# Kernel tuning notes

Measured on AMD Instinct MI355X. Metric: run time of the kernel, lower is better.

## Reference

```python
import jax, jax.numpy as jnp
import numpy as np

B, N, C = 2, 384, 1024          # images, proposals/image, box_head feature dim
H_REPN = 256                    # RePN hidden
G_HID, HEADS = 256, 4           # GATConv hidden / heads
TOPK = 8
IMG_H, IMG_W = 800, 800
NEG_SLOPE = 0.2                 # PyG GATConv leaky_relu default


def _box_geom(bx):
    # normalized [x, y, w, h], matching _box_geom
    scale = jnp.array([IMG_W, IMG_H, IMG_W, IMG_H], dtype=bx.dtype)
    nb = bx / scale
    return jnp.stack([nb[:, 0], nb[:, 1], nb[:, 2] - nb[:, 0], nb[:, 3] - nb[:, 1]], axis=1)


def _gat_layer(x, src, tgt, W, att_src, att_dst, bias, heads, out_c):
    # PyG GATConv: messages flow src -> tgt, softmax over incoming edges at tgt
    n = x.shape[0]
    xw = (x @ W).reshape(n, heads, out_c)               # [N, H, F]
    a_s = jnp.sum(xw * att_src, axis=-1)                # [N, H]
    a_d = jnp.sum(xw * att_dst, axis=-1)                # [N, H]
    e = jax.nn.leaky_relu(a_s[src] + a_d[tgt], NEG_SLOPE)  # [E, H]
    e_max = jax.ops.segment_max(e, tgt, num_segments=n)    # stable softmax per target
    alpha = jnp.exp(e - e_max[tgt])
    denom = jax.ops.segment_sum(alpha, tgt, num_segments=n)
    alpha = alpha / jnp.maximum(denom, 1e-16)[tgt]          # [E, H]
    out = jax.ops.segment_sum(xw[src] * alpha[..., None], tgt, num_segments=n)
    return out.reshape(n, heads * out_c) + bias


def setup_inputs() -> dict:
    key = jax.random.key(0)
    ks = jax.random.split(key, 16)
    feats = jax.random.normal(ks[0], (B, N, C), dtype=jnp.float32)
    # boxes with x1<x2, y1<y2 inside the image
    xy = jax.random.uniform(ks[1], (B, N, 2), minval=0.0, maxval=650.0)
    wh = jax.random.uniform(ks[2], (B, N, 2), minval=10.0, maxval=150.0)
    boxes = jnp.concatenate([xy, xy + wh], axis=-1).astype(jnp.float32)
    s = 0.02
    params = {
        'fc1_w': jax.random.normal(ks[3], (2 * C + 4, H_REPN)) * s,
        'fc1_b': jnp.zeros((H_REPN,), jnp.float32),
        'fc2_w': jax.random.normal(ks[4], (H_REPN, 1)) * s,
        'fc2_b': jnp.zeros((1,), jnp.float32),
        'gat1_w': jax.random.normal(ks[5], (C + 4, HEADS * G_HID)) * s,
        'gat1_att_src': jax.random.normal(ks[6], (HEADS, G_HID)) * s,
        'gat1_att_dst': jax.random.normal(ks[7], (HEADS, G_HID)) * s,
        'gat1_b': jnp.zeros((HEADS * G_HID,), jnp.float32),
        'gat2_w': jax.random.normal(ks[8], (HEADS * G_HID, 2)) * s,
        'gat2_att_src': jax.random.normal(ks[9], (1, 2)) * s,
        'gat2_att_dst': jax.random.normal(ks[10], (1, 2)) * s,
        'gat2_b': jnp.zeros((2,), jnp.float32),
    }
    return {'feats': feats, 'boxes': boxes, **params}


def reference(feats, boxes, fc1_w, fc1_b, fc2_w, fc2_b,
              gat1_w, gat1_att_src, gat1_att_dst, gat1_b,
              gat2_w, gat2_att_src, gat2_att_dst, gat2_b):
    def single(f, bx):
        geom4 = _box_geom(bx)                               # [N, 4]
        x = jnp.concatenate([f, geom4], axis=1)             # [N, C+4]
        # RelationProposalNetwork: fc1(cat[f_i, f_j, |b_i-b_j|]) done as split matmuls
        Wa, Wb, Wg = fc1_w[:C], fc1_w[C:2 * C], fc1_w[2 * C:]
        p1 = f @ Wa                                         # [N, H]
        p2 = f @ Wb                                         # [N, H]
        gdiff = jnp.abs(bx[:, None, :] - bx[None, :, :])    # [N, N, 4]
        h = jax.nn.relu(p1[:, None, :] + p2[None, :, :] + gdiff @ Wg + fc1_b)
        rel = (h @ fc2_w)[..., 0] + fc2_b[0]                # [N, N]
        # _make_edge_index: mask diagonal, top-k per row; edge = [dst_node, neighbor]
        rn = rel - jnp.eye(N, dtype=rel.dtype) * 1e6
        nbr = jax.lax.top_k(rn, TOPK)[1]                    # [N, k]
        src = jnp.repeat(jnp.arange(N), TOPK)               # edge_index[0] (PyG source)
        tgt = nbr.reshape(-1)                               # edge_index[1] (PyG target)
        loop = jnp.arange(N)                                # GATConv add_self_loops=True
        src = jnp.concatenate([src, loop])
        tgt = jnp.concatenate([tgt, loop])
        h1 = jax.nn.relu(_gat_layer(x, src, tgt, gat1_w, gat1_att_src, gat1_att_dst, gat1_b, HEADS, G_HID))
        logits = _gat_layer(h1, src, tgt, gat2_w, gat2_att_src, gat2_att_dst, gat2_b, 1, 2)
        return logits                                       # [N, 2]
    return jax.vmap(single)(feats, boxes)
```

## Files before the change

### kernel.cpp

```cpp
#include <hip/hip_runtime.h>

#define BB 2
#define NN 384
#define CC 1024
#define HR 256
#define NHEADS 4
#define TOPK 8
#define CAP 448
#define NEG 0.2f

typedef __attribute__((ext_vector_type(8))) short bf16x8;
typedef __attribute__((ext_vector_type(4))) float f32x4;

__device__ __forceinline__ unsigned short f2bf(float v) {
    unsigned u = __float_as_uint(v);
    return (unsigned short)((u + 0x7FFFu + ((u >> 16) & 1u)) >> 16);
}
__device__ __forceinline__ float bf2f(unsigned short h) {
    return __uint_as_float((unsigned)h << 16);
}

__global__ __launch_bounds__(256) void k_prep(const float* __restrict__ feats,
        const float* __restrict__ boxes, const float* __restrict__ gat1_w,
        const float* __restrict__ fc1_w,
        uint4* __restrict__ Asw, uint4* __restrict__ Bsw,
        uint4* __restrict__ Ah, uint4* __restrict__ Al,
        uint4* __restrict__ Bh, uint4* __restrict__ Bl,
        float4* __restrict__ wgp, int* __restrict__ counts,
        float* __restrict__ xw2) {
    __shared__ float sw[32][65];
    int blk = blockIdx.x;
    int t = threadIdx.x;
    int gflat = blk * 256 + t;
    if (gflat < BB * NN) counts[gflat] = 0;
    if (gflat < BB * NN * 2) xw2[gflat] = 0.f;

    if (blk < 396) {
        int flat = gflat;
        int lane = flat & 63;
        int kc = (flat >> 6) % 33;
        int mt = flat / (33 * 64);
        int m = mt * 16 + (lane & 15);
        int k0 = kc * 32 + (lane >> 4) * 8;
        unsigned short vals[8];
        const float s = 1.0f / 800.0f;
#pragma unroll
        for (int j = 0; j < 8; j++) {
            int k = k0 + j;
            float v;
            if (k < CC) v = feats[(size_t)m * CC + k];
            else if (k < CC + 4) {
                const float* bx = boxes + (size_t)m * 4;
                int gk = k - CC;
                v = (gk == 0) ? bx[0] * s : (gk == 1) ? bx[1] * s
                  : (gk == 2) ? (bx[2] - bx[0]) * s : (bx[3] - bx[1]) * s;
            } else v = 0.f;
            vals[j] = f2bf(v);
        }
        uint4 pk;
        pk.x = (unsigned)vals[0] | ((unsigned)vals[1] << 16);
        pk.y = (unsigned)vals[2] | ((unsigned)vals[3] << 16);
        pk.z = (unsigned)vals[4] | ((unsigned)vals[5] << 16);
        pk.w = (unsigned)vals[6] | ((unsigned)vals[7] << 16);
        Asw[flat] = pk;
    } else if (blk < 924) {
        int blkrel = blk - 396;
        int ntg = blkrel / 33;
        int kc  = blkrel % 33;
        int k0 = kc * 32;
        int n0 = ntg * 64;
#pragma unroll
        for (int pass = 0; pass < 8; pass++) {
            int kl = pass * 4 + (t >> 6);
            int k = k0 + kl;
            int nl = t & 63;
            float v = (k < CC + 4) ? gat1_w[(size_t)k * 1024 + n0 + nl] : 0.f;
            sw[kl][nl] = v;
        }
        __syncthreads();
        int local_nt = t >> 6;
        int lane = t & 63;
        int nn = lane & 15;
        int q = lane >> 4;
        int nl = local_nt * 16 + nn;
        unsigned short vals[8];
#pragma unroll
        for (int j = 0; j < 8; j++) vals[j] = f2bf(sw[q * 8 + j][nl]);
        uint4 pk;
        pk.x = (unsigned)vals[0] | ((unsigned)vals[1] << 16);
        pk.y = (unsigned)vals[2] | ((unsigned)vals[3] << 16);
        pk.z = (unsigned)vals[4] | ((unsigned)vals[5] << 16);
        pk.w = (unsigned)vals[6] | ((unsigned)vals[7] << 16);
        int nt = ntg * 4 + local_nt;
        Bsw[(size_t)nt * 33 * 64 + kc * 64 + lane] = pk;
    } else if (blk < 1308) {
        int flat = gflat - 924 * 256;
        int lane = flat & 63;
        int kc = (flat >> 6) % 32;
        int mt = flat / (32 * 64);
        int m = mt * 16 + (lane & 15);
        int k0 = kc * 32 + (lane >> 4) * 8;
        unsigned short vh[8], vl[8];
        const float* src = feats + (size_t)m * CC + k0;
#pragma unroll
        for (int j = 0; j < 8; j++) {
            float v = src[j];
            unsigned short h = f2bf(v);
            vh[j] = h;
            vl[j] = f2bf(v - bf2f(h));
        }
        uint4 ph, pl;
        ph.x = (unsigned)vh[0] | ((unsigned)vh[1] << 16);
        ph.y = (unsigned)vh[2] | ((unsigned)vh[3] << 16);
        ph.z = (unsigned)vh[4] | ((unsigned)vh[5] << 16);
        ph.w = (unsigned)vh[6] | ((unsigned)vh[7] << 16);
        pl.x = (unsigned)vl[0] | ((unsigned)vl[1] << 16);
        pl.y = (unsigned)vl[2] | ((unsigned)vl[3] << 16);
        pl.z = (unsigned)vl[4] | ((unsigned)vl[5] << 16);
        pl.w = (unsigned)vl[6] | ((unsigned)vl[7] << 16);
        Ah[flat] = ph; Al[flat] = pl;
    } else if (blk < 1564) {
        int blkrel = blk - 1308;
        int ntg = blkrel / 32;
        int kc  = blkrel % 32;
        int k0 = kc * 32;
        int n0 = ntg * 64;
#pragma unroll
        for (int pass = 0; pass < 8; pass++) {
            int kl = pass * 4 + (t >> 6);
            int k = k0 + kl;
            int n = n0 + (t & 63);
            float v = (n < 256) ? fc1_w[(size_t)k * 256 + n]
                                : fc1_w[(size_t)(CC + k) * 256 + (n - 256)];
            sw[kl][t & 63] = v;
        }
        __syncthreads();
        int local_nt = t >> 6;
        int lane = t & 63;
        int nn = lane & 15;
        int q = lane >> 4;
        int nl = local_nt * 16 + nn;
        unsigned short vh[8], vl[8];
#pragma unroll
        for (int j = 0; j < 8; j++) {
            float v = sw[q * 8 + j][nl];
            unsigned short h = f2bf(v);
            vh[j] = h;
            vl[j] = f2bf(v - bf2f(h));
        }
        uint4 ph, pl;
        ph.x = (unsigned)vh[0] | ((unsigned)vh[1] << 16);
        ph.y = (unsigned)vh[2] | ((unsigned)vh[3] << 16);
        ph.z = (unsigned)vh[4] | ((unsigned)vh[5] << 16);
        ph.w = (unsigned)vh[6] | ((unsigned)vh[7] << 16);
        pl.x = (unsigned)vl[0] | ((unsigned)vl[1] << 16);
        pl.y = (unsigned)vl[2] | ((unsigned)vl[3] << 16);
        pl.z = (unsigned)vl[4] | ((unsigned)vl[5] << 16);
        pl.w = (unsigned)vl[6] | ((unsigned)vl[7] << 16);
        int nt = ntg * 4 + local_nt;
        size_t o = (size_t)nt * 32 * 64 + kc * 64 + lane;
        Bh[o] = ph; Bl[o] = pl;
    } else {
        int c = t;
        float4 w;
        w.x = fc1_w[(size_t)(2 * CC + 0) * HR + c];
        w.y = fc1_w[(size_t)(2 * CC + 1) * HR + c];
        w.z = fc1_w[(size_t)(2 * CC + 2) * HR + c];
        w.w = fc1_w[(size_t)(2 * CC + 3) * HR + c];
        wgp[c] = w;
    }
}

__global__ __launch_bounds__(512) void k_mm(const uint4* __restrict__ Ah,
        const uint4* __restrict__ Al, const uint4* __restrict__ Bh,
        const uint4* __restrict__ Bl, const float* __restrict__ fc1_b,
        float* __restrict__ p1, float* __restrict__ p2t,
        const uint4* __restrict__ Asw, const uint4* __restrict__ Bsw,
        float* __restrict__ xw1) {
    __shared__ float lds[4][64][8];
    int t = threadIdx.x;
    int w = t >> 6;
    int lane = t & 63;
    int g = w & 3;
    int kh = w >> 2;
    int blk0 = blockIdx.x;
    if (blk0 < 192) {
        int mtp = blk0 >> 3;
        int nt = (blk0 & 7) * 4 + g;
        int mt0 = mtp * 2;
        f32x4 acc0 = {0.f, 0.f, 0.f, 0.f};
        f32x4 acc1 = {0.f, 0.f, 0.f, 0.f};
        const uint4* pah0 = Ah + (size_t)mt0 * 32 * 64 + (size_t)kh * 16 * 64 + lane;
        const uint4* pal0 = Al + (size_t)mt0 * 32 * 64 + (size_t)kh * 16 * 64 + lane;
        const uint4* pbh = Bh + (size_t)nt * 32 * 64 + (size_t)kh * 16 * 64 + lane;
        const uint4* pbl = Bl + (size_t)nt * 32 * 64 + (size_t)kh * 16 * 64 + lane;
#pragma unroll 2
        for (int kc = 0; kc < 16; kc++) {
            uint4 ah0 = pah0[kc * 64];
            uint4 al0 = pal0[kc * 64];
            uint4 ah1 = pah0[kc * 64 + 2048];
            uint4 al1 = pal0[kc * 64 + 2048];
            uint4 bh = pbh[kc * 64];
            uint4 bl = pbl[kc * 64];
            acc0 = __builtin_amdgcn_mfma_f32_16x16x32_bf16(*(bf16x8*)&ah0, *(bf16x8*)&bh, acc0, 0, 0, 0);
            acc0 = __builtin_amdgcn_mfma_f32_16x16x32_bf16(*(bf16x8*)&ah0, *(bf16x8*)&bl, acc0, 0, 0, 0);
            acc0 = __builtin_amdgcn_mfma_f32_16x16x32_bf16(*(bf16x8*)&al0, *(bf16x8*)&bh, acc0, 0, 0, 0);
            acc1 = __builtin_amdgcn_mfma_f32_16x16x32_bf16(*(bf16x8*)&ah1, *(bf16x8*)&bh, acc1, 0, 0, 0);
            acc1 = __builtin_amdgcn_mfma_f32_16x16x32_bf16(*(bf16x8*)&ah1, *(bf16x8*)&bl, acc1, 0, 0, 0);
            acc1 = __builtin_amdgcn_mfma_f32_16x16x32_bf16(*(bf16x8*)&al1, *(bf16x8*)&bh, acc1, 0, 0, 0);
        }
        if (kh == 1) {
#pragma unroll
            for (int r = 0; r < 4; r++) { lds[g][lane][r] = acc0[r]; lds[g][lane][4 + r] = acc1[r]; }
        }
        __syncthreads();
        if (kh == 0) {
#pragma unroll
            for (int r = 0; r < 4; r++) { acc0[r] += lds[g][lane][r]; acc1[r] += lds[g][lane][4 + r]; }
            int col = nt * 16 + (lane & 15);
            int rbase = (lane >> 4) * 4;
            if (col < 256) {
                float bias = fc1_b[col];
#pragma unroll
                for (int r = 0; r < 4; r++) {
                    p1[(size_t)(mt0 * 16 + rbase + r) * 256 + col] = acc0[r] + bias;
                    p1[(size_t)(mt0 * 16 + 16 + rbase + r) * 256 + col] = acc1[r] + bias;
                }
            } else {
#pragma unroll
                for (int r = 0; r < 4; r++) {
                    int rr0 = mt0 * 16 + rbase + r;
                    int rr1 = rr0 + 16;
                    p2t[((size_t)(rr0 / NN) * 256 + (col - 256)) * NN + (rr0 % NN)] = acc0[r];
                    p2t[((size_t)(rr1 / NN) * 256 + (col - 256)) * NN + (rr1 % NN)] = acc1[r];
                }
            }
        }
    } else {
        int blk = blk0 - 192;
        int mtp = blk >> 4;
        int nt = (blk & 15) * 4 + g;
        int mt0 = mtp * 2;
        int nk = kh ? 16 : 17;
        f32x4 acc0 = {0.f, 0.f, 0.f, 0.f};
        f32x4 acc1 = {0.f, 0.f, 0.f, 0.f};
        const uint4* pa0 = Asw + (size_t)mt0 * 33 * 64 + (size_t)kh * 17 * 64 + lane;
        const uint4* pb = Bsw + (size_t)nt * 33 * 64 + (size_t)kh * 17 * 64 + lane;
#pragma unroll 4
        for (int kc = 0; kc < nk; kc++) {
            uint4 a0 = pa0[kc * 64];
            uint4 a1 = pa0[kc * 64 + 2112];
            uint4 bv = pb[kc * 64];
            acc0 = __builtin_amdgcn_mfma_f32_16x16x32_bf16(*(bf16x8*)&a0, *(bf16x8*)&bv, acc0, 0, 0, 0);
            acc1 = __builtin_amdgcn_mfma_f32_16x16x32_bf16(*(bf16x8*)&a1, *(bf16x8*)&bv, acc1, 0, 0, 0);
        }
        if (kh == 1) {
#pragma unroll
            for (int r = 0; r < 4; r++) { lds[g][lane][r] = acc0[r]; lds[g][lane][4 + r] = acc1[r]; }
        }
        __syncthreads();
        if (kh == 0) {
#pragma unroll
            for (int r = 0; r < 4; r++) { acc0[r] += lds[g][lane][r]; acc1[r] += lds[g][lane][4 + r]; }
            int col = nt * 16 + (lane & 15);
            int rbase = (lane >> 4) * 4;
#pragma unroll
            for (int r = 0; r < 4; r++) {
                xw1[(size_t)(mt0 * 16 + rbase + r) * 1024 + col] = acc0[r];
                xw1[(size_t)(mt0 * 16 + 16 + rbase + r) * 1024 + col] = acc1[r];
            }
        }
    }
}

__global__ __launch_bounds__(384) void k_relatt(const float* __restrict__ p1,
        const float* __restrict__ p2t, const float* __restrict__ boxes,
        const float4* __restrict__ wgp, const float* __restrict__ fc2_w,
        float* __restrict__ rel_a, float* __restrict__ rel_b,
        const float* __restrict__ xw1, const float* __restrict__ att_src,
        const float* __restrict__ att_dst, float* __restrict__ a_s,
        float* __restrict__ a_d) {
    int blk0 = blockIdx.x;
    if (blk0 < 768) {
        int blk = blk0;
        int p = blk >> 1;
        int ch = blk & 1;
        int b = p / (NN / 2);
        int i0 = (p - b * (NN / 2)) * 2;
        int row0 = b * NN + i0;
        int j = threadIdx.x;
        float a0 = boxes[(size_t)row0 * 4 + 0];
        float a1 = boxes[(size_t)row0 * 4 + 1];
        float a2 = boxes[(size_t)row0 * 4 + 2];
        float a3 = boxes[(size_t)row0 * 4 + 3];
        float c0 = boxes[(size_t)(row0 + 1) * 4 + 0];
        float c1 = boxes[(size_t)(row0 + 1) * 4 + 1];
        float c2 = boxes[(size_t)(row0 + 1) * 4 + 2];
        float c3 = boxes[(size_t)(row0 + 1) * 4 + 3];
        float4 bj = *(const float4*)(boxes + ((size_t)b * NN + j) * 4);
        float g00 = fabsf(a0 - bj.x), g01 = fabsf(a1 - bj.y);
        float g02 = fabsf(a2 - bj.z), g03 = fabsf(a3 - bj.w);
        float g10 = fabsf(c0 - bj.x), g11 = fabsf(c1 - bj.y);
        float g12 = fabsf(c2 - bj.z), g13 = fabsf(c3 - bj.w);
        const float* p1r0 = p1 + (size_t)row0 * HR + ch * 128;
        const float* p1r1 = p1r0 + HR;
        const float* p2b = p2t + (size_t)b * HR * NN + (size_t)ch * 128 * NN + j;
        const float4* wg = wgp + ch * 128;
        const float* w2 = fc2_w + ch * 128;
        float acc0 = 0.f, acc1 = 0.f;
#pragma unroll 8
        for (int c = 0; c < 128; c++) {
            float4 w = wg[c];
            float pa = p1r0[c];
            float pb = p1r1[c];
            float wc = w2[c];
            float p2v = p2b[(size_t)c * NN];
            float v0 = pa + p2v + g00 * w.x + g01 * w.y + g02 * w.z + g03 * w.w;
            float v1 = pb + p2v + g10 * w.x + g11 * w.y + g12 * w.z + g13 * w.w;
            acc0 += fmaxf(v0, 0.f) * wc;
            acc1 += fmaxf(v1, 0.f) * wc;
        }
        float* dst = ch ? rel_b : rel_a;
        dst[(size_t)row0 * NN + j] = acc0;
        dst[(size_t)(row0 + 1) * NN + j] = acc1;
    } else {
        int node = blk0 - 768;
        int t = threadIdx.x;
        if (t >= 256) return;
        int w = t >> 6;
        int lane = t & 63;
        const float4* xr = (const float4*)(xw1 + (size_t)node * 1024 + w * 256);
        const float4* sr = (const float4*)(att_src + w * 256);
        const float4* dr = (const float4*)(att_dst + w * 256);
        float4 x = xr[lane];
        float4 s = sr[lane];
        float4 d = dr[lane];
        float ps = x.x * s.x + x.y * s.y + x.z * s.z + x.w * s.w;
        float pd = x.x * d.x + x.y * d.y + x.z * d.z + x.w * d.w;
#pragma unroll
        for (int off = 32; off > 0; off >>= 1) {
            ps += __shfl_xor(ps, off);
            pd += __shfl_xor(pd, off);
        }
        if (lane == 0) {
            a_s[(size_t)node * NHEADS + w] = ps;
            a_d[(size_t)node * NHEADS + w] = pd;
        }
    }
}

__global__ __launch_bounds__(64) void k_topk_inv(const float* __restrict__ rel_a,
        const float* __restrict__ rel_b, int* __restrict__ counts,
        int* __restrict__ inlist) {
    int row = blockIdx.x;
    int b = row / NN;
    int i = row - b * NN;
    int t = threadIdx.x;
    const float* ra = rel_a + (size_t)row * NN;
    const float* rb = rel_b + (size_t)row * NN;
    float v[6]; int id[6];
#pragma unroll
    for (int q = 0; q < 6; q++) {
        int j = t + q * 64;
        float val = ra[j] + rb[j];
        if (j == i) val = -INFINITY;
        v[q] = val; id[q] = j;
    }
    int mine = -1;
    for (int k = 0; k < TOPK; k++) {
        float bv = -INFINITY; int bi = NN;
#pragma unroll
        for (int q = 0; q < 6; q++) {
            if (v[q] > bv || (v[q] == bv && id[q] < bi)) { bv = v[q]; bi = id[q]; }
        }
        for (int off = 32; off > 0; off >>= 1) {
            float ov = __shfl_down(bv, off);
            int   oi = __shfl_down(bi, off);
            if (ov > bv || (ov == bv && oi < bi)) { bv = ov; bi = oi; }
        }
        bi = __shfl(bi, 0);
        if (t == k) mine = bi;
#pragma unroll
        for (int q = 0; q < 6; q++) if (id[q] == bi) v[q] = -INFINITY;
    }
    if (t < TOPK) {
        int tg = b * NN + mine;
        int q = atomicAdd(&counts[tg], 1);
        inlist[(size_t)tg * CAP + q] = i;
    } else if (t == TOPK) {
        int q = atomicAdd(&counts[row], 1);
        inlist[(size_t)row * CAP + q] = i;
    }
}

__global__ __launch_bounds__(256) void k_agg1h(const int* __restrict__ counts,
        const int* __restrict__ inlist, const float* __restrict__ a_s,
        const float* __restrict__ a_d, const float* __restrict__ xw1,
        const float* __restrict__ gat1_b, const float* __restrict__ w2,
        float* __restrict__ xw2) {
    __shared__ int slist[CAP];
    __shared__ float walpha[CAP];
    __shared__ float redp[8];
    int blk = blockIdx.x;
    int node = blk >> 2;
    int h = blk & 3;
    int b = node / NN;
    int t = threadIdx.x;
    int wid = t >> 6;
    int lane = t & 63;
    int deg = counts[node];
    for (int e = t; e < deg; e += 256) slist[e] = inlist[(size_t)node * CAP + e];
    __syncthreads();
    if (t < 64) {
        float ad = a_d[(size_t)node * NHEADS + h];
        float vals[7];
        int cnt = 0;
        float vmax = -INFINITY;
        for (int e = t; e < deg; e += 64) {
            float x = a_s[(size_t)(b * NN + slist[e]) * NHEADS + h] + ad;
            x = x >= 0.f ? x : NEG * x;
            vals[cnt++] = x;
            vmax = fmaxf(vmax, x);
        }
#pragma unroll
        for (int off = 32; off > 0; off >>= 1)
            vmax = fmaxf(vmax, __shfl_xor(vmax, off));
        float sum = 0.f;
        for (int i = 0; i < cnt; i++) {
            vals[i] = expf(vals[i] - vmax);
            sum += vals[i];
        }
#pragma unroll
        for (int off = 32; off > 0; off >>= 1)
            sum += __shfl_xor(sum, off);
        float inv = 1.f / fmaxf(sum, 1e-16f);
        cnt = 0;
        for (int e = t; e < deg; e += 64) walpha[e] = vals[cnt++] * inv;
    }
    __syncthreads();
    float acc = 0.f;
    for (int e = 0; e < deg; e++)
        acc += walpha[e] * xw1[(size_t)(b * NN + slist[e]) * 1024 + h * 256 + t];
    float o = fmaxf(acc + gat1_b[h * 256 + t], 0.f);
    int d = h * 256 + t;
    float p0 = o * w2[d * 2];
    float p1v = o * w2[d * 2 + 1];
#pragma unroll
    for (int off = 32; off > 0; off >>= 1) {
        p0 += __shfl_xor(p0, off);
        p1v += __shfl_xor(p1v, off);
    }
    if (lane == 0) { redp[wid] = p0; redp[4 + wid] = p1v; }
    __syncthreads();
    if (t == 0) {
        atomicAdd(&xw2[(size_t)node * 2],     redp[0] + redp[1] + redp[2] + redp[3]);
        atomicAdd(&xw2[(size_t)node * 2 + 1], redp[4] + redp[5] + redp[6] + redp[7]);
    }
}

__global__ __launch_bounds__(64) void k_agg2(const int* __restrict__ counts,
        const int* __restrict__ inlist, const float* __restrict__ xw2,
        const float* __restrict__ as2, const float* __restrict__ ad2,
        const float* __restrict__ b2, float* __restrict__ out) {
    int node = blockIdx.x;
    int b = node / NN;
    int lane = threadIdx.x;
    int deg = counts[node];
    float s0 = as2[0], s1 = as2[1];
    float d0 = ad2[0], d1 = ad2[1];
    float2 xwn = *(const float2*)(xw2 + (size_t)node * 2);
    float ad = xwn.x * d0 + xwn.y * d1;
    float vals[7], xs0[7], xs1[7];
    int cnt = 0;
    float vmax = -INFINITY;
    for (int e = lane; e < deg; e += 64) {
        int s = b * NN + inlist[(size_t)node * CAP + e];
        float2 xws = *(const float2*)(xw2 + (size_t)s * 2);
        float x = xws.x * s0 + xws.y * s1 + ad;
        x = x >= 0.f ? x : NEG * x;
        xs0[cnt] = xws.x; xs1[cnt] = xws.y; vals[cnt] = x; cnt++;
        vmax = fmaxf(vmax, x);
    }
#pragma unroll
    for (int off = 32; off > 0; off >>= 1)
        vmax = fmaxf(vmax, __shfl_xor(vmax, off));
    float sum = 0.f;
    for (int i = 0; i < cnt; i++) {
        vals[i] = expf(vals[i] - vmax);
        sum += vals[i];
    }
#pragma unroll
    for (int off = 32; off > 0; off >>= 1)
        sum += __shfl_xor(sum, off);
    float inv = 1.f / fmaxf(sum, 1e-16f);
    float a0 = 0.f, a1 = 0.f;
    for (int i = 0; i < cnt; i++) {
        a0 += vals[i] * xs0[i];
        a1 += vals[i] * xs1[i];
    }
#pragma unroll
    for (int off = 32; off > 0; off >>= 1) {
        a0 += __shfl_xor(a0, off);
        a1 += __shfl_xor(a1, off);
    }
    if (lane == 0) {
        out[(size_t)node * 2]     = a0 * inv + b2[0];
        out[(size_t)node * 2 + 1] = a1 * inv + b2[1];
    }
}

extern "C" void kernel_launch(void* const* d_in, const int* in_sizes, int n_in,
                              void* d_out, int out_size, void* d_ws, size_t ws_size,
                              hipStream_t stream) {
    const float* feats  = (const float*)d_in[0];
    const float* boxes  = (const float*)d_in[1];
    const float* fc1_w  = (const float*)d_in[2];
    const float* fc1_b  = (const float*)d_in[3];
    const float* fc2_w  = (const float*)d_in[4];
    const float* fc2_b  = (const float*)d_in[5];
    const float* gat1_w = (const float*)d_in[6];
    const float* g1as   = (const float*)d_in[7];
    const float* g1ad   = (const float*)d_in[8];
    const float* gat1_b = (const float*)d_in[9];
    const float* gat2_w = (const float*)d_in[10];
    const float* g2as   = (const float*)d_in[11];
    const float* g2ad   = (const float*)d_in[12];
    const float* gat2_b = (const float*)d_in[13];
    float* out = (float*)d_out;
    (void)fc2_b;

    char* ws = (char*)d_ws;
    size_t off = 0;
    auto alloc = [&](size_t bytes) -> void* {
        void* p = ws + off;
        off += (bytes + 255) / 256 * 256;
        return p;
    };
    int*   counts = (int*)alloc((size_t)BB * NN * 4);
    int*   inlist = (int*)alloc((size_t)BB * NN * CAP * 4);
    float* p1     = (float*)alloc((size_t)BB * NN * HR * 4);
    float* p2t    = (float*)alloc((size_t)BB * HR * NN * 4);
    float* rel_a  = (float*)alloc((size_t)BB * NN * NN * 4);
    float* rel_b  = (float*)alloc((size_t)BB * NN * NN * 4);
    float* xw1    = (float*)alloc((size_t)BB * NN * 1024 * 4);
    float* a_s1   = (float*)alloc((size_t)BB * NN * NHEADS * 4);
    float* a_d1   = (float*)alloc((size_t)BB * NN * NHEADS * 4);
    float* xw2    = (float*)alloc((size_t)BB * NN * 2 * 4);
    uint4* Asw    = (uint4*)alloc((size_t)48 * 33 * 64 * 16);
    uint4* Bsw    = (uint4*)alloc((size_t)64 * 33 * 64 * 16);
    uint4* Ah     = (uint4*)alloc((size_t)48 * 32 * 64 * 16);
    uint4* Al     = (uint4*)alloc((size_t)48 * 32 * 64 * 16);
    uint4* Bh     = (uint4*)alloc((size_t)32 * 32 * 64 * 16);
    uint4* Bl     = (uint4*)alloc((size_t)32 * 32 * 64 * 16);
    float4* wgp   = (float4*)alloc((size_t)HR * 16);
    (void)ws_size; (void)in_sizes; (void)n_in; (void)out_size;

    k_prep<<<1565, 256, 0, stream>>>(feats, boxes, gat1_w, fc1_w,
                                     Asw, Bsw, Ah, Al, Bh, Bl, wgp, counts, xw2);
    k_mm<<<576, 512, 0, stream>>>(Ah, Al, Bh, Bl, fc1_b, p1, p2t, Asw, Bsw, xw1);
    k_relatt<<<1536, 384, 0, stream>>>(p1, p2t, boxes, wgp, fc2_w, rel_a, rel_b,
                                       xw1, g1as, g1ad, a_s1, a_d1);
    k_topk_inv<<<BB * NN, 64, 0, stream>>>(rel_a, rel_b, counts, inlist);
    k_agg1h<<<BB * NN * NHEADS, 256, 0, stream>>>(counts, inlist, a_s1, a_d1, xw1,
                                                  gat1_b, gat2_w, xw2);
    k_agg2<<<BB * NN, 64, 0, stream>>>(counts, inlist, xw2, g2as, g2ad, gat2_b, out);
}
```

Before: 161.6 us.

## Fuse relation scoring with per-row top-k selection and inverse edge list build

Merges the relation score kernel and the top-k kernel. Each block now computes both channel halves for two rows and runs a block-wide top-k using wave shuffles plus shared-memory reduction, then appends edges atomically. This removes the rel_a/rel_b global round trip and one kernel launch. In exchange, the relation blocks are halved in count and each does twice the serial work, and the top-k needs 16 block barriers per block, which reduces parallelism.

```diff
diff --git a/kernel.cpp b/kernel.cpp
--- a/kernel.cpp
+++ b/kernel.cpp
@@ -273,22 +273,27 @@
     }
 }
 
-__global__ __launch_bounds__(384) void k_relatt(const float* __restrict__ p1,
+__global__ __launch_bounds__(384) void k_relattk(const float* __restrict__ p1,
         const float* __restrict__ p2t, const float* __restrict__ boxes,
         const float4* __restrict__ wgp, const float* __restrict__ fc2_w,
-        float* __restrict__ rel_a, float* __restrict__ rel_b,
         const float* __restrict__ xw1, const float* __restrict__ att_src,
         const float* __restrict__ att_dst, float* __restrict__ a_s,
-        float* __restrict__ a_d) {
+        float* __restrict__ a_d, int* __restrict__ counts,
+        int* __restrict__ inlist) {
     int blk0 = blockIdx.x;
-    if (blk0 < 768) {
-        int blk = blk0;
-        int p = blk >> 1;
-        int ch = blk & 1;
+    if (blk0 < 384) {
+        __shared__ float swv[6];
+        __shared__ int   swi[6];
+        __shared__ int   swin;
+        __shared__ int   win[8];
+        int p = blk0;
         int b = p / (NN / 2);
         int i0 = (p - b * (NN / 2)) * 2;
         int row0 = b * NN + i0;
-        int j = threadIdx.x;
+        int t = threadIdx.x;
+        int j = t;
+        int wid = t >> 6;
+        int lane = t & 63;
         float a0 = boxes[(size_t)row0 * 4 + 0];
         float a1 = boxes[(size_t)row0 * 4 + 1];
         float a2 = boxes[(size_t)row0 * 4 + 2];
@@ -302,29 +307,86 @@
         float g02 = fabsf(a2 - bj.z), g03 = fabsf(a3 - bj.w);
         float g10 = fabsf(c0 - bj.x), g11 = fabsf(c1 - bj.y);
         float g12 = fabsf(c2 - bj.z), g13 = fabsf(c3 - bj.w);
-        const float* p1r0 = p1 + (size_t)row0 * HR + ch * 128;
-        const float* p1r1 = p1r0 + HR;
-        const float* p2b = p2t + (size_t)b * HR * NN + (size_t)ch * 128 * NN + j;
-        const float4* wg = wgp + ch * 128;
-        const float* w2 = fc2_w + ch * 128;
-        float acc0 = 0.f, acc1 = 0.f;
+        float acc00 = 0.f, acc10 = 0.f;
+        {
+            const float* p1r0 = p1 + (size_t)row0 * HR;
+            const float* p1r1 = p1r0 + HR;
+            const float* p2b = p2t + (size_t)b * HR * NN + j;
+            const float4* wg = wgp;
+            const float* w2 = fc2_w;
 #pragma unroll 8
-        for (int c = 0; c < 128; c++) {
-            float4 w = wg[c];
-            float pa = p1r0[c];
-            float pb = p1r1[c];
-            float wc = w2[c];
-            float p2v = p2b[(size_t)c * NN];
-            float v0 = pa + p2v + g00 * w.x + g01 * w.y + g02 * w.z + g03 * w.w;
-            float v1 = pb + p2v + g10 * w.x + g11 * w.y + g12 * w.z + g13 * w.w;
-            acc0 += fmaxf(v0, 0.f) * wc;
-            acc1 += fmaxf(v1, 0.f) * wc;
-        }
-        float* dst = ch ? rel_b : rel_a;
-        dst[(size_t)row0 * NN + j] = acc0;
-        dst[(size_t)(row0 + 1) * NN + j] = acc1;
+            for (int c = 0; c < 128; c++) {
+                float4 w = wg[c];
+                float pa = p1r0[c];
+                float pb = p1r1[c];
+                float wc = w2[c];
+                float p2v = p2b[(size_t)c * NN];
+                float v0 = pa + p2v + g00 * w.x + g01 * w.y + g02 * w.z + g03 * w.w;
+                float v1 = pb + p2v + g10 * w.x + g11 * w.y + g12 * w.z + g13 * w.w;
+                acc00 += fmaxf(v0, 0.f) * wc;
+                acc10 += fmaxf(v1, 0.f) * wc;
+            }
+        }
+        float acc01 = 0.f, acc11 = 0.f;
+        {
+            const float* p1r0 = p1 + (size_t)row0 * HR + 128;
+            const float* p1r1 = p1r0 + HR;
+            const float* p2b = p2t + (size_t)b * HR * NN + (size_t)128 * NN + j;
+            const float4* wg = wgp + 128;
+            const float* w2 = fc2_w + 128;
+#pragma unroll 8
+            for (int c = 0; c < 128; c++) {
+                float4 w = wg[c];
+                float pa = p1r0[c];
+                float pb = p1r1[c];
+                float wc = w2[c];
+                float p2v = p2b[(size_t)c * NN];
+                float v0 = pa + p2v + g00 * w.x + g01 * w.y + g02 * w.z + g03 * w.w;
+                float v1 = pb + p2v + g10 * w.x + g11 * w.y + g12 * w.z + g13 * w.w;
+                acc01 += fmaxf(v0, 0.f) * wc;
+                acc11 += fmaxf(v1, 0.f) * wc;
+            }
+        }
+        float val0 = acc00 + acc01;
+        float val1 = acc10 + acc11;
+        for (int r = 0; r < 2; r++) {
+            int i = i0 + r;
+            float v = r ? val1 : val0;
+            if (j == i) v = -INFINITY;
+            int id = j;
+            for (int k = 0; k < TOPK; k++) {
+                float bv = v; int bi = id;
+#pragma unroll
+                for (int off = 32; off > 0; off >>= 1) {
+                    float ov = __shfl_down(bv, off);
+                    int   oi = __shfl_down(bi, off);
+                    if (ov > bv || (ov == bv && oi < bi)) { bv = ov; bi = oi; }
+                }
+                if (lane == 0) { swv[wid] = bv; swi[wid] = bi; }
+                __syncthreads();
+                if (t == 0) {
+                    float cv = swv[0]; int ci = swi[0];
+#pragma unroll
+                    for (int q = 1; q < 6; q++) {
+                        if (swv[q] > cv || (swv[q] == cv && swi[q] < ci)) { cv = swv[q]; ci = swi[q]; }
+                    }
+                    swin = ci; win[k] = ci;
+                }
+                __syncthreads();
+                if (id == swin) v = -INFINITY;
+            }
+            if (t < TOPK) {
+                int tg = b * NN + win[t];
+                int q = atomicAdd(&counts[tg], 1);
+                inlist[(size_t)tg * CAP + q] = i;
+            } else if (t == TOPK) {
+                int row = b * NN + i;
+                int q = atomicAdd(&counts[row], 1);
+                inlist[(size_t)row * CAP + q] = i;
+            }
+        }
     } else {
-        int node = blk0 - 768;
+        int node = blk0 - 384;
         int t = threadIdx.x;
         if (t >= 256) return;
         int w = t >> 6;
@@ -346,50 +408,6 @@
             a_s[(size_t)node * NHEADS + w] = ps;
             a_d[(size_t)node * NHEADS + w] = pd;
         }
-    }
-}
-
-__global__ __launch_bounds__(64) void k_topk_inv(const float* __restrict__ rel_a,
-        const float* __restrict__ rel_b, int* __restrict__ counts,
-        int* __restrict__ inlist) {
-    int row = blockIdx.x;
-    int b = row / NN;
-    int i = row - b * NN;
-    int t = threadIdx.x;
-    const float* ra = rel_a + (size_t)row * NN;
-    const float* rb = rel_b + (size_t)row * NN;
-    float v[6]; int id[6];
-#pragma unroll
-    for (int q = 0; q < 6; q++) {
-        int j = t + q * 64;
-        float val = ra[j] + rb[j];
-        if (j == i) val = -INFINITY;
-        v[q] = val; id[q] = j;
-    }
-    int mine = -1;
-    for (int k = 0; k < TOPK; k++) {
-        float bv = -INFINITY; int bi = NN;
-#pragma unroll
-        for (int q = 0; q < 6; q++) {
-            if (v[q] > bv || (v[q] == bv && id[q] < bi)) { bv = v[q]; bi = id[q]; }
-        }
-        for (int off = 32; off > 0; off >>= 1) {
-            float ov = __shfl_down(bv, off);
-            int   oi = __shfl_down(bi, off);
-            if (ov > bv || (ov == bv && oi < bi)) { bv = ov; bi = oi; }
-        }
-        bi = __shfl(bi, 0);
-        if (t == k) mine = bi;
-#pragma unroll
-        for (int q = 0; q < 6; q++) if (id[q] == bi) v[q] = -INFINITY;
-    }
-    if (t < TOPK) {
-        int tg = b * NN + mine;
-        int q = atomicAdd(&counts[tg], 1);
-        inlist[(size_t)tg * CAP + q] = i;
-    } else if (t == TOPK) {
-        int q = atomicAdd(&counts[row], 1);
-        inlist[(size_t)row * CAP + q] = i;
     }
 }
 
@@ -540,8 +558,6 @@
     int*   inlist = (int*)alloc((size_t)BB * NN * CAP * 4);
     float* p1     = (float*)alloc((size_t)BB * NN * HR * 4);
     float* p2t    = (float*)alloc((size_t)BB * HR * NN * 4);
-    float* rel_a  = (float*)alloc((size_t)BB * NN * NN * 4);
-    float* rel_b  = (float*)alloc((size_t)BB * NN * NN * 4);
     float* xw1    = (float*)alloc((size_t)BB * NN * 1024 * 4);
     float* a_s1   = (float*)alloc((size_t)BB * NN * NHEADS * 4);
     float* a_d1   = (float*)alloc((size_t)BB * NN * NHEADS * 4);
@@ -558,9 +574,8 @@
     k_prep<<<1565, 256, 0, stream>>>(feats, boxes, gat1_w, fc1_w,
                                      Asw, Bsw, Ah, Al, Bh, Bl, wgp, counts, xw2);
     k_mm<<<576, 512, 0, stream>>>(Ah, Al, Bh, Bl, fc1_b, p1, p2t, Asw, Bsw, xw1);
-    k_relatt<<<1536, 384, 0, stream>>>(p1, p2t, boxes, wgp, fc2_w, rel_a, rel_b,
-                                       xw1, g1as, g1ad, a_s1, a_d1);
-    k_topk_inv<<<BB * NN, 64, 0, stream>>>(rel_a, rel_b, counts, inlist);
+    k_relattk<<<1152, 384, 0, stream>>>(p1, p2t, boxes, wgp, fc2_w,
+                                        xw1, g1as, g1ad, a_s1, a_d1, counts, inlist);
     k_agg1h<<<BB * NN * NHEADS, 256, 0, stream>>>(counts, inlist, a_s1, a_d1, xw1,
                                                   gat1_b, gat2_w, xw2);
     k_agg2<<<BB * NN, 64, 0, stream>>>(counts, inlist, xw2, g2as, g2ad, gat2_b, out);
```

After: 178.0 us. +10.1%, slower.
